# Kernel tuning notes

Hardware: AMD Instinct MI355X
Metric: run time of the kernel (lower is better)

## Reference

```python
import jax, jax.numpy as jnp
from jax import lax
import numpy as np

N_HARMONICS = 8      # matches init_kwargs N
CC_ITERS = 500       # kornia.contrib.connected_components(num_iterations=500)


def _connected_components(mask):
    # kornia-style label propagation: init labels = linear index, bg = 0,
    # iterate 3x3 max-pool restricted to foreground pixels.
    B, C, H, W = mask.shape
    fg = mask == 1.0
    init = jnp.arange(B * C * H * W, dtype=jnp.float32).reshape(B, C, H, W)
    init = jnp.where(fg, init, 0.0)

    def body(_, out):
        pooled = lax.reduce_window(out, -jnp.inf, lax.max,
                                   (1, 1, 3, 3), (1, 1, 1, 1),
                                   ((0, 0), (0, 0), (1, 1), (1, 1)))
        return jnp.where(fg, pooled, out)

    return lax.fori_loop(0, CC_ITERS, body, init)


@jax.jit
def _find_contours(img):
    # img: [B,1,H,W] binary float
    p = jnp.pad(img, ((0, 0), (0, 0), (1, 1), (1, 1)))
    cc = _connected_components(p)[:, :, 1:-1, 1:-1]
    k = jnp.array([[1., 1., 1.], [1., -8., 1.], [1., 1., 1.]], jnp.float32)[None, None]
    conv = lax.conv_general_dilated(p, k, (1, 1), ((1, 1), (1, 1)),
                                    dimension_numbers=('NCHW', 'OIHW', 'NCHW'))
    boundary = (conv < 0).astype(jnp.float32)[:, :, 1:-1, 1:-1]
    return boundary * cc  # labeled contour image


def _components_np(img, N):
    # Per unique label (incl. 0, exactly as torch.unique does): sort points by
    # polar angle about their centroid, compute Fourier amplitudes A[1..N].
    centers, amps = [], []
    for lab in np.unique(img):
        pts = np.argwhere(img == lab).astype(np.float32)  # (row, col), row-major like torch.nonzero
        c = pts.mean(axis=0)
        ang = np.arctan2(pts[:, 1] - c[1], pts[:, 0] - c[0])
        pts = pts[np.argsort(ang, kind='stable')]
        p2 = np.roll(pts, -1, axis=0)
        d1 = np.sqrt((pts[:, 1] - c[1]) ** 2 + (pts[:, 0] - c[0]) ** 2)
        d2 = np.sqrt((p2[:, 1] - c[1]) ** 2 + (p2[:, 0] - c[0]) ** 2)
        delta = d1 - d2
        d3 = np.sqrt(((pts - p2) ** 2).sum(-1))
        l = np.cumsum(d3)
        L = l[-1] if l[-1] != 0 else 1.0
        nz = delta != 0
        k = np.arange(1, N + 1, dtype=np.float32)[:, None]          # [N,1]
        ph = 2.0 * np.pi * k * l[nz][None, :] / L                    # [N,M]
        a = (delta[nz][None] * np.sin(ph)).sum(-1) / (k[:, 0] * np.pi)
        b = -(delta[nz][None] * np.cos(ph)).sum(-1) / (k[:, 0] * np.pi)
        amps.append(np.sqrt(a * a + b * b).astype(np.float32))
        centers.append(c)
    return np.stack(centers), np.stack(amps)


def _pairs(pred_c, tgt_c, N):
    # Geometry preprocessing (integer coords -> constants): per batch item,
    # amplitudes for pred/gt objects plus nearest-centroid matching.
    out = []
    for b in range(pred_c.shape[0]):
        pi, ti = pred_c[b, 0], tgt_c[b, 0]
        if ti.sum() == 0 or pi.sum() == 0:
            out.append(None)
            continue
        p_cent, pA = _components_np(pi, N)
        g_cent, gA = _components_np(ti, N)
        if g_cent.shape[0] <= p_cent.shape[0]:
            d = np.linalg.norm(g_cent[:, None] - p_cent[None], axis=-1)
            out.append((pA, gA, d.argmin(axis=1), True))
        else:
            d = np.linalg.norm(p_cent[:, None] - g_cent[None], axis=-1)
            out.append((pA, gA, d.argmin(axis=1), False))
    return out


def _loss_from_pairs(pairs, weight):
    scale = 0.5 * weight ** 2
    shift = jnp.log(1.0 + weight ** 2)
    total = jnp.zeros((), jnp.float32)
    for pr in pairs:
        if pr is None:
            continue
        pA, gA, m, gt_le = pr
        pd = jnp.asarray(pA) * scale + shift
        gd = jnp.asarray(gA) * scale + shift
        diff = jnp.abs(pd[m] - gd) if gt_le else jnp.abs(gd[m] - pd)
        total = total + diff.sum()
    return total


def setup_inputs() -> dict:
    key = jax.random.key(0)
    B, H, W = 2, 512, 512
    base = np.zeros((H, W), np.float32)
    for i in range(8):
        for j in range(8):
            base[20 + i * 60:56 + i * 60, 20 + j * 60:56 + j * 60] = 1.0
    target = np.broadcast_to(base, (B, 1, H, W)).copy()
    pred_mask = np.stack([np.roll(base, 3 * (b + 1), axis=1) for b in range(B)])[:, None]
    noise = np.asarray(jax.random.normal(key, (B, 1, H, W), jnp.float32))
    pred = 4.0 * pred_mask - 2.0 + 0.05 * noise  # logits; never flips threshold
    return {"pred": jnp.asarray(pred, jnp.float32),
            "target": jnp.asarray(target, jnp.float32),
            "weight": jnp.ones((), jnp.float32)}


def reference(pred, target, weight):
    predm = (jax.nn.sigmoid(pred) > 0.5).astype(jnp.float32)
    if target.ndim == 3:
        target = target[:, None]
    pc = np.asarray(_find_contours(predm))
    tc = np.asarray(_find_contours(target))
    pairs = _pairs(pc, tc, N_HARMONICS)
    return _loss_from_pairs(pairs, weight)
```

## Files before the change

### kernel.cpp

```cpp
#include <hip/hip_runtime.h>
#include <cstdint>
#include <cstddef>

#pragma clang fp contract(off)

#define DEVFN __device__ __forceinline__

constexpr int H = 512, W = 512, HW = H * W;
constexpr int NIMG = 4;
constexpr int PADW = 514;
constexpr int PADHW = PADW * PADW;
constexpr int MAXC = 128;
constexpr int NH = 8;
constexpr int PADCAP = 2 * HW;
constexpr int LEAFCAP = 6144;
constexpr int BMW = 16520;
constexpr int PROP_ITERS = 6;
constexpr int TILE = 2048;
constexpr int PSTRIDE = HW + 4 * MAXC;

constexpr float TWOPIF = (float)(2.0 * 3.14159265358979323846);
constexpr float PIF    = (float)(3.14159265358979323846);

struct Ptrs {
  const float* pred; const float* tgt; const float* wgt; float* out;
  int *labA, *labB, *cid;
  unsigned *pts, *sortPts, *bitmap;
  unsigned long long *keys;
  int *lablist, *counts, *offs, *aoffs, *poffs, *plog, *ptot, *ncomp;
  int *RC, *mcnt, *leafCnt, *leafBase, *leafTot, *leaves, *mergecnt;
  float *dpt, *sortD, *Lval, *centers, *leafSums, *amps;
  float2 *pair;
  float2 *nz;
};

DEVFN int point_search(const int* offs, int nc, int p) {
  int lo = 0, hi = nc - 1;
  while (lo < hi) { int mid = (lo + hi + 1) >> 1; if (offs[mid] <= p) lo = mid; else hi = mid - 1; }
  return lo;
}
DEVFN int seg_search(const int* poffs, const int* plog, int nc, int s) {
  int lo = 0, hi = nc - 1;
  while (lo < hi) { int mid = (lo + hi + 1) >> 1; if (poffs[mid] <= s) lo = mid; else hi = mid - 1; }
  if (s < poffs[lo] + (1 << plog[lo])) return lo;
  return -1;
}

__global__ void k_init(Ptrs w) {
  int idx = blockIdx.x * blockDim.x + threadIdx.x;
  if (idx >= NIMG * HW) return;
  int img = idx / HW, p = idx % HW, r = p / W, c = p % W;
  bool fg;
  if (img < 2) fg = w.pred[img * HW + p] > 0.0f;
  else         fg = (w.tgt[(img - 2) * HW + p] == 1.0f);
  int b = img & 1;
  w.labA[idx] = fg ? (b * PADHW + (r + 1) * PADW + (c + 1)) : 0;
}

__global__ void k_prop(const int* src, int* dst) {
  int idx = blockIdx.x * blockDim.x + threadIdx.x;
  if (idx >= NIMG * HW) return;
  int img = idx / HW, p = idx % HW, r = p / W, c = p % W;
  const int* s = src + img * HW;
  int own = s[p];
  if (own <= 0) { dst[idx] = own; return; }
  int best = own;
  for (int dr = -1; dr <= 1; dr++)
    for (int dc = -1; dc <= 1; dc++) {
      int rr = r + dr, cc2 = c + dc;
      if (rr < 0 || rr >= H || cc2 < 0 || cc2 >= W) continue;
      int v = s[rr * W + cc2];
      if (v > best) best = v;
    }
  int b = img & 1;
  int rel = best - b * PADHW;
  int qr = rel / PADW - 1, qc = rel % PADW - 1;
  int v2 = s[qr * W + qc];
  if (v2 > best) best = v2;
  dst[idx] = best;
}

__global__ void k_contour(Ptrs w) {
  int idx = blockIdx.x * blockDim.x + threadIdx.x;
  if (idx >= NIMG * HW) return;
  int img = idx / HW, p = idx % HW, r = p / W, c = p % W;
  const int* lab = w.labA + img * HW;
  int lv = lab[p];
  int outv = 0;
  if (lv > 0) {
    bool bg = false;
    for (int dr = -1; dr <= 1 && !bg; dr++)
      for (int dc = -1; dc <= 1; dc++) {
        if (dr == 0 && dc == 0) continue;
        int rr = r + dr, cc2 = c + dc;
        bool nfg = (rr >= 0 && rr < H && cc2 >= 0 && cc2 < W) ? (lab[rr * W + cc2] > 0) : false;
        if (!nfg) { bg = true; break; }
      }
    if (bg) outv = lv;
  }
  w.labB[idx] = outv;
}

__global__ void k_bitmap(Ptrs w) {
  int idx = blockIdx.x * blockDim.x + threadIdx.x;
  if (idx >= NIMG * HW) return;
  int img = idx / HW;
  int v = w.labB[idx];
  int lane = threadIdx.x & 63;
  int prev = __shfl_up(v, 1);
  if (lane == 0 || v != prev)
    atomicOr(&w.bitmap[img * BMW + (v >> 5)], 1u << (v & 31));
}

__global__ void k_collect(Ptrs w) {
  int idx = blockIdx.x * blockDim.x + threadIdx.x;
  if (idx >= NIMG * BMW) return;
  int img = idx / BMW, wd = idx % BMW;
  unsigned bits = w.bitmap[img * BMW + wd];
  while (bits) {
    int b = __ffs(bits) - 1;
    bits &= bits - 1;
    int slot = atomicAdd(&w.ncomp[img], 1);
    if (slot < MAXC) w.lablist[img * MAXC + slot] = wd * 32 + b;
  }
}
__global__ void k_sortlab(Ptrs w) {
  int img = threadIdx.x; if (img >= NIMG) return;
  int nc = w.ncomp[img];
  if (nc > MAXC) { nc = MAXC; w.ncomp[img] = MAXC; }
  int* ll = w.lablist + img * MAXC;
  for (int a = 1; a < nc; a++) {
    int v = ll[a]; int b = a - 1;
    while (b >= 0 && ll[b] > v) { ll[b + 1] = ll[b]; b--; }
    ll[b + 1] = v;
  }
}

__global__ void k_cid(Ptrs w) {
  int idx = blockIdx.x * blockDim.x + threadIdx.x;
  if (idx >= NIMG * HW) return;
  int img = idx / HW;
  int v = w.labB[idx];
  const int* ll = w.lablist + img * MAXC;
  int nc = w.ncomp[img];
  int lo = 0, hi = nc - 1, c = 0;
  while (lo <= hi) {
    int mid = (lo + hi) >> 1; int lv = ll[mid];
    if (lv == v) { c = mid; break; }
    if (lv < v) lo = mid + 1; else hi = mid - 1;
  }
  w.cid[idx] = c;
}

__global__ void k_rowcount(Ptrs w) {
  __shared__ int cnt[64 * MAXC];
  int t = threadIdx.x;
  int rowg = blockIdx.x * 64 + t;
  for (int j = 0; j < MAXC; j++) cnt[t * MAXC + j] = 0;
  int img = rowg / H, r = rowg % H;
  for (int c = 0; c < W; c++) cnt[t * MAXC + w.cid[img * HW + r * W + c]]++;
  for (int j = 0; j < MAXC; j++) w.RC[rowg * MAXC + j] = cnt[t * MAXC + j];
}
__global__ void k_colsum(Ptrs w) {
  int idx = blockIdx.x * blockDim.x + threadIdx.x;
  if (idx >= NIMG * MAXC) return;
  int img = idx / MAXC, comp = idx % MAXC;
  const int* rcp = w.RC + (size_t)img * H * MAXC + comp;
  int s = 0;
  #pragma unroll 8
  for (int r = 0; r < H; r++) s += rcp[(size_t)r * MAXC];
  w.counts[img * MAXC + comp] = s;
}
__global__ void k_offsets(Ptrs w) {
  int img = threadIdx.x; if (img >= NIMG) return;
  int nc = w.ncomp[img];
  int* offs  = w.offs  + img * (MAXC + 1);
  int* aoffs = w.aoffs + img * (MAXC + 1);
  int* poffs = w.poffs + img * (MAXC + 1);
  int* plog  = w.plog  + img * MAXC;
  const int* counts = w.counts + img * MAXC;
  int acc = 0, po = 0, ao = 0;
  for (int c = 0; c < nc; c++) {
    offs[c] = acc; acc += counts[c];
    aoffs[c] = ao; ao += (counts[c] + 3) & ~3;
    int n = counts[c];
    int lg = 0; while ((1 << lg) < n) lg++;
    int P = 1 << lg;
    po = (po + P - 1) & ~(P - 1);
    poffs[c] = po; plog[c] = lg; po += P;
  }
  offs[nc] = acc; aoffs[nc] = ao; poffs[nc] = po;
  w.ptot[img] = po;
}
__global__ void k_rowscan(Ptrs w) {
  int idx = blockIdx.x * blockDim.x + threadIdx.x;
  if (idx >= NIMG * MAXC) return;
  int img = idx / MAXC, comp = idx % MAXC;
  if (comp >= w.ncomp[img]) return;
  int base = w.offs[img * (MAXC + 1) + comp];
  for (int r = 0; r < H; r++) {
    int row = img * H + r;
    int tmp = w.RC[row * MAXC + comp];
    w.RC[row * MAXC + comp] = base;
    base += tmp;
  }
}
__global__ void k_scatter(Ptrs w) {
  __shared__ int run[64 * MAXC];
  int t = threadIdx.x;
  int rowg = blockIdx.x * 64 + t;
  for (int j = 0; j < MAXC; j++) run[t * MAXC + j] = w.RC[rowg * MAXC + j];
  int img = rowg / H, r = rowg % H;
  float* planeR = (float*)w.labA + img * HW;
  float* planeC = (float*)w.labB + img * HW;
  for (int c = 0; c < W; c++) {
    int v = w.cid[img * HW + r * W + c];
    int pos = run[t * MAXC + v]++;
    w.pts[img * HW + pos] = ((unsigned)r << 16) | (unsigned)c;
    planeR[pos] = (float)r;
    planeC[pos] = (float)c;
  }
}

__global__ __launch_bounds__(192, 1) void k_mean(Ptrs w) {
  __shared__ alignas(16) float rbuf[2][TILE];
  __shared__ alignas(16) float cbuf[2][TILE];
  int bid = blockIdx.x;
  int img = bid / MAXC, comp = bid % MAXC;
  if (comp >= w.ncomp[img]) return;
  int n = w.counts[img * MAXC + comp];
  int base = w.offs[img * (MAXC + 1) + comp];
  const float* srcR = (const float*)w.labA + img * HW + base;
  const float* srcC = (const float*)w.labB + img * HW + base;
  int t = threadIdx.x;
  int ntile = (n + TILE - 1) / TILE;

  auto fill = [&](int tl, int bb, int lo, int step) {
    int tb = tl * TILE;
    int len = n - tb; if (len > TILE) len = TILE;
    for (int j = lo; j < len; j += step) {
      rbuf[bb][j] = srcR[tb + j];
      cbuf[bb][j] = srcC[tb + j];
    }
  };

  fill(0, 0, t, 192);
  __syncthreads();
  float s = 0.f;
  for (int tl = 0; tl < ntile; tl++) {
    int bb = tl & 1;
    if (t >= 64 && tl + 1 < ntile) fill(tl + 1, bb ^ 1, t - 64, 128);
    if (t < 2) {
      const float*  fb = (t == 0) ? &rbuf[bb][0] : &cbuf[bb][0];
      const float4* b4 = (const float4*)fb;
      int len = n - tl * TILE; if (len > TILE) len = TILE;
      int nb = len >> 6;
      for (int b = 0; b < nb; b++) {
        const float4* _s = b4 + (size_t)b * 16;
        float4 A0=_s[0],A1=_s[1],A2=_s[2],A3=_s[3],A4=_s[4],A5=_s[5],A6=_s[6],A7=_s[7];
        float4 A8=_s[8],A9=_s[9],A10=_s[10],A11=_s[11],A12=_s[12],A13=_s[13],A14=_s[14],A15=_s[15];
        s=s+A0.x; s=s+A0.y; s=s+A0.z; s=s+A0.w;  s=s+A1.x; s=s+A1.y; s=s+A1.z; s=s+A1.w;
        s=s+A2.x; s=s+A2.y; s=s+A2.z; s=s+A2.w;  s=s+A3.x; s=s+A3.y; s=s+A3.z; s=s+A3.w;
        s=s+A4.x; s=s+A4.y; s=s+A4.z; s=s+A4.w;  s=s+A5.x; s=s+A5.y; s=s+A5.z; s=s+A5.w;
        s=s+A6.x; s=s+A6.y; s=s+A6.z; s=s+A6.w;  s=s+A7.x; s=s+A7.y; s=s+A7.z; s=s+A7.w;
        s=s+A8.x; s=s+A8.y; s=s+A8.z; s=s+A8.w;  s=s+A9.x; s=s+A9.y; s=s+A9.z; s=s+A9.w;
        s=s+A10.x;s=s+A10.y;s=s+A10.z;s=s+A10.w; s=s+A11.x;s=s+A11.y;s=s+A11.z;s=s+A11.w;
        s=s+A12.x;s=s+A12.y;s=s+A12.z;s=s+A12.w; s=s+A13.x;s=s+A13.y;s=s+A13.z;s=s+A13.w;
        s=s+A14.x;s=s+A14.y;s=s+A14.z;s=s+A14.w; s=s+A15.x;s=s+A15.y;s=s+A15.z;s=s+A15.w;
      }
      for (int j = nb << 6; j < len; j++) s = s + fb[j];
    }
    __syncthreads();
  }
  float sr = __shfl(s, 0);
  float sc = __shfl(s, 1);
  if (t == 0) {
    w.centers[(img * MAXC + comp) * 2 + 0] = (float)((double)sr / (double)n);
    w.centers[(img * MAXC + comp) * 2 + 1] = (float)((double)sc / (double)n);
  }
}

__global__ void k_keys(Ptrs w) {
  int idx = blockIdx.x * blockDim.x + threadIdx.x;
  if (idx >= NIMG * PADCAP) return;
  int img = idx / PADCAP, s = idx % PADCAP;
  unsigned long long key = ~0ULL;
  int nc = w.ncomp[img];
  const int* poffs = w.poffs + img * (MAXC + 1);
  const int* plog  = w.plog  + img * MAXC;
  if (s < w.ptot[img]) {
    int comp = seg_search(poffs, plog, nc, s);
    if (comp >= 0) {
      int li = s - poffs[comp];
      int n = w.counts[img * MAXC + comp];
      if (li < n) {
        int pbase = w.offs[img * (MAXC + 1) + comp];
        unsigned u = w.pts[img * HW + pbase + li];
        float rowf = (float)(u >> 16), colf = (float)(u & 0xFFFFu);
        float cr = w.centers[(img * MAXC + comp) * 2 + 0];
        float cc = w.centers[(img * MAXC + comp) * 2 + 1];
        float dy = colf - cc;
        float dx = rowf - cr;
        float ang = (float)atan2((double)dy, (double)dx);
        float q1 = dy * dy;
        float q2 = dx * dx;
        float ss = q1 + q2;
        w.dpt[img * HW + pbase + li] = sqrtf(ss);
        unsigned bits = __float_as_uint(ang);
        unsigned k32 = (bits & 0x80000000u) ? ~bits : (bits | 0x80000000u);
        key = ((unsigned long long)k32 << 32) | (unsigned)li;
      }
    }
  }
  w.keys[img * PADCAP + s] = key;
}

__global__ void k_bitonic_local(Ptrs w, int mode, int sizeLog) {
  __shared__ unsigned long long sk[2048];
  __shared__ int   sli[2048];
  __shared__ short scomp[2048];
  __shared__ short spl[2048];
  int tilesPerImg = PADCAP / 2048;
  int img = blockIdx.x / tilesPerImg;
  int tb = (blockIdx.x % tilesPerImg) * 2048;
  int pt = w.ptot[img];
  if (tb >= pt) return;
  const int* poffs = w.poffs + img * (MAXC + 1);
  const int* plog  = w.plog  + img * MAXC;
  int nc = w.ncomp[img];
  for (int u = threadIdx.x; u < 2048; u += blockDim.x) {
    int s = tb + u;
    sk[u] = w.keys[img * PADCAP + s];
    int comp = (s < pt) ? seg_search(poffs, plog, nc, s) : -1;
    scomp[u] = (short)comp;
    spl[u] = comp >= 0 ? (short)plog[comp] : (short)-1;
    sli[u] = comp >= 0 ? s - poffs[comp] : 0;
  }
  __syncthreads();
  int t = threadIdx.x;
  int slLo, slHi;
  if (mode == 0) { slLo = 1; slHi = 11; } else { slLo = sizeLog; slHi = sizeLog; }
  for (int sl = slLo; sl <= slHi; sl++) {
    int size = 1 << sl;
    int stTop = (mode == 0) ? (sl - 1) : 10;
    for (int st = stTop; st >= 0; st--) {
      int stride = 1 << st;
      int i = ((t >> st) << (st + 1)) | (t & (stride - 1));
      int j = i + stride;
      if (scomp[i] >= 0 && scomp[i] == scomp[j] && sl <= spl[i]) {
        bool asc = ((sli[i] & size) == 0);
        if ((sk[i] > sk[j]) == asc) {
          unsigned long long tmp = sk[i]; sk[i] = sk[j]; sk[j] = tmp;
        }
      }
      __syncthreads();
    }
  }
  for (int u = threadIdx.x; u < 2048; u += blockDim.x) w.keys[img * PADCAP + tb + u] = sk[u];
}

__global__ void k_bitonic_global(Ptrs w, int sizeLog, int strideLog) {
  int idx = blockIdx.x * blockDim.x + threadIdx.x;
  const int half = 1 << 17;
  if (idx >= NIMG * half) return;
  int img = idx / half, tt = idx % half;
  int stride = 1 << strideLog;
  int i = ((tt >> strideLog) << (strideLog + 1)) | (tt & (stride - 1));
  int j = i + stride;
  int pt = w.ptot[img];
  if (i >= pt) return;
  const int* poffs = w.poffs + img * (MAXC + 1);
  const int* plog  = w.plog  + img * MAXC;
  int nc = w.ncomp[img];
  int ci = seg_search(poffs, plog, nc, i);
  int cj = (j < pt) ? seg_search(poffs, plog, nc, j) : -1;
  if (ci < 0 || ci != cj) return;
  if (sizeLog > plog[ci]) return;
  bool asc = (((i - poffs[ci]) & (1 << sizeLog)) == 0);
  unsigned long long a = w.keys[img * PADCAP + i];
  unsigned long long b = w.keys[img * PADCAP + j];
  if ((a > b) == asc) {
    w.keys[img * PADCAP + i] = b;
    w.keys[img * PADCAP + j] = a;
  }
}

__global__ void k_gather_sorted(Ptrs w) {
  int idx = blockIdx.x * blockDim.x + threadIdx.x;
  if (idx >= NIMG * HW) return;
  int img = idx / HW, p = idx % HW;
  const int* offs = w.offs + img * (MAXC + 1);
  int comp = point_search(offs, w.ncomp[img], p);
  int li = p - offs[comp];
  int slot = w.poffs[img * (MAXC + 1) + comp] + li;
  unsigned long long key = w.keys[img * PADCAP + slot];
  int rank = (int)(unsigned)(key & 0xFFFFFFFFULL);
  w.sortPts[idx] = w.pts[img * HW + offs[comp] + rank];
  w.sortD[idx]   = w.dpt[img * HW + offs[comp] + rank];
}

__global__ void k_delta(Ptrs w) {
  int idx = blockIdx.x * blockDim.x + threadIdx.x;
  if (idx >= NIMG * HW) return;
  int img = idx / HW, p = idx % HW;
  const int* offs = w.offs + img * (MAXC + 1);
  int comp = point_search(offs, w.ncomp[img], p);
  int li = p - offs[comp];
  int n = w.counts[img * MAXC + comp];
  int jn = (li + 1 < n) ? (p + 1) : offs[comp];
  int jn_abs = img * HW + jn;
  float dlt = w.sortD[idx] - w.sortD[jn_abs];
  unsigned u = w.sortPts[idx], v = w.sortPts[jn_abs];
  float dr = (float)(int)(u >> 16) - (float)(int)(v >> 16);
  float dc = (float)(int)(u & 0xFFFFu) - (float)(int)(v & 0xFFFFu);
  float q1 = dr * dr;
  float q2 = dc * dc;
  float ss = q1 + q2;
  int ai = img * PSTRIDE + w.aoffs[img * (MAXC + 1) + comp] + li;
  w.pair[ai] = make_float2(sqrtf(ss), dlt);
}

__global__ __launch_bounds__(256, 1) void k_cumsum(Ptrs w) {
  __shared__ alignas(16) float dbuf[3][TILE];
  __shared__ alignas(16) float tbuf[3][TILE];
  __shared__ alignas(16) float lbuf[2][TILE];
  int bid = blockIdx.x;
  int img = bid / MAXC, comp = bid % MAXC;
  if (comp >= w.ncomp[img]) return;
  int n = w.counts[img * MAXC + comp];
  int base = w.offs[img * (MAXC + 1) + comp];
  int abase = w.aoffs[img * (MAXC + 1) + comp];
  const float2* pr = w.pair + (size_t)img * PSTRIDE + abase;
  float2* nzp = w.nz + img * HW + base;
  int t = threadIdx.x;
  int lane3 = t - 192;
  int ntile = (n + TILE - 1) / TILE;
  float l = 0.f;
  int mcur = 0;

  auto fill = [&](int tl, int lo, int step) {
    int cb = tl % 3;
    int tb = tl * TILE;
    int len = n - tb; if (len > TILE) len = TILE;
    const float2* src = pr + tb;
    for (int j = lo; j < len; j += step) {
      float2 p = src[j];
      dbuf[cb][j] = p.x;
      tbuf[cb][j] = p.y;
    }
  };

  auto compact = [&](int tlc) {
    int cb = tlc % 3, lb = tlc & 1;
    int tb = tlc * TILE;
    int len = n - tb; if (len > TILE) len = TILE;
    const float* tv = tbuf[cb];
    const float* lv = lbuf[lb];
    int nblk = (len + 63) >> 6;
    for (int b = 0; b < nblk; b++) {
      int j = (b << 6) + lane3;
      float dv = (j < len) ? tv[j] : 0.0f;
      bool nz = (j < len) && (dv != 0.0f);
      unsigned long long mask = __ballot(nz);
      int pos = mcur + __popcll(mask & ((1ull << lane3) - 1ull));
      if (nz) nzp[pos] = make_float2(dv, lv[j]);
      mcur += __popcll(mask);
    }
  };

  fill(0, t, 256);
  __syncthreads();
  for (int tl = 0; tl < ntile; tl++) {
    int cb = tl % 3;
    if (t >= 64 && t < 192) {
      if (tl + 1 < ntile) fill(tl + 1, t - 64, 128);
    } else if (t == 0) {
      int len = n - tl * TILE; if (len > TILE) len = TILE;
      const float4* d4 = (const float4*)&dbuf[cb][0];
      float*  lbr = lbuf[tl & 1];
      float4* lb4 = (float4*)lbr;
      int nb = len >> 6;
      for (int b = 0; b < nb; b++) {
        const float4* _s = d4 + (size_t)b * 16;
        float4 A0=_s[0],A1=_s[1],A2=_s[2],A3=_s[3],A4=_s[4],A5=_s[5],A6=_s[6],A7=_s[7];
        float4 A8=_s[8],A9=_s[9],A10=_s[10],A11=_s[11],A12=_s[12],A13=_s[13],A14=_s[14],A15=_s[15];
        float4* _d = lb4 + (size_t)b * 16;
        float4 L;
        l=l+A0.x; L.x=l; l=l+A0.y; L.y=l; l=l+A0.z; L.z=l; l=l+A0.w; L.w=l; _d[0]=L;
        l=l+A1.x; L.x=l; l=l+A1.y; L.y=l; l=l+A1.z; L.z=l; l=l+A1.w; L.w=l; _d[1]=L;
        l=l+A2.x; L.x=l; l=l+A2.y; L.y=l; l=l+A2.z; L.z=l; l=l+A2.w; L.w=l; _d[2]=L;
        l=l+A3.x; L.x=l; l=l+A3.y; L.y=l; l=l+A3.z; L.z=l; l=l+A3.w; L.w=l; _d[3]=L;
        l=l+A4.x; L.x=l; l=l+A4.y; L.y=l; l=l+A4.z; L.z=l; l=l+A4.w; L.w=l; _d[4]=L;
        l=l+A5.x; L.x=l; l=l+A5.y; L.y=l; l=l+A5.z; L.z=l; l=l+A5.w; L.w=l; _d[5]=L;
        l=l+A6.x; L.x=l; l=l+A6.y; L.y=l; l=l+A6.z; L.z=l; l=l+A6.w; L.w=l; _d[6]=L;
        l=l+A7.x; L.x=l; l=l+A7.y; L.y=l; l=l+A7.z; L.z=l; l=l+A7.w; L.w=l; _d[7]=L;
        l=l+A8.x; L.x=l; l=l+A8.y; L.y=l; l=l+A8.z; L.z=l; l=l+A8.w; L.w=l; _d[8]=L;
        l=l+A9.x; L.x=l; l=l+A9.y; L.y=l; l=l+A9.z; L.z=l; l=l+A9.w; L.w=l; _d[9]=L;
        l=l+A10.x; L.x=l; l=l+A10.y; L.y=l; l=l+A10.z; L.z=l; l=l+A10.w; L.w=l; _d[10]=L;
        l=l+A11.x; L.x=l; l=l+A11.y; L.y=l; l=l+A11.z; L.z=l; l=l+A11.w; L.w=l; _d[11]=L;
        l=l+A12.x; L.x=l; l=l+A12.y; L.y=l; l=l+A12.z; L.z=l; l=l+A12.w; L.w=l; _d[12]=L;
        l=l+A13.x; L.x=l; l=l+A13.y; L.y=l; l=l+A13.z; L.z=l; l=l+A13.w; L.w=l; _d[13]=L;
        l=l+A14.x; L.x=l; l=l+A14.y; L.y=l; l=l+A14.z; L.z=l; l=l+A14.w; L.w=l; _d[14]=L;
        l=l+A15.x; L.x=l; l=l+A15.y; L.y=l; l=l+A15.z; L.z=l; l=l+A15.w; L.w=l; _d[15]=L;
      }
      for (int j = nb << 6; j < len; j++) {
        l = l + dbuf[cb][j];
        lbr[j] = l;
      }
    } else if (t >= 192 && tl > 0) {
      compact(tl - 1);
    }
    __syncthreads();
  }
  if (t >= 192) compact(ntile - 1);
  if (t == 192) w.mcnt[img * MAXC + comp] = mcur;
  if (t == 0)  w.Lval[img * MAXC + comp] = (l != 0.0f) ? l : 1.0f;
}

__global__ __launch_bounds__(128) void k_leafcount(Ptrs w) {
  __shared__ int sN[40][128];
  int img = blockIdx.x;
  int t = threadIdx.x, comp = t;
  if (comp >= w.ncomp[img]) return;
  int m = w.mcnt[img * MAXC + comp];
  int cnt = 0;
  if (m > 0) {
    int sp = 0, n = m;
    for (;;) {
      while (n > 128) { int n2 = n / 2; n2 -= n2 % 8; sN[sp][t] = n - n2; sp++; n = n2; }
      cnt++;
      if (sp == 0) break;
      sp--; n = sN[sp][t];
    }
  }
  w.leafCnt[img * MAXC + comp] = cnt;
}
__global__ void k_leafscan(Ptrs w) {
  int img = threadIdx.x; if (img >= NIMG) return;
  int nc = w.ncomp[img];
  int base = 0;
  for (int c = 0; c < nc; c++) {
    w.leafBase[img * MAXC + c] = base;
    base += w.leafCnt[img * MAXC + c];
  }
  w.leafTot[img] = base <= LEAFCAP ? base : LEAFCAP;
}
__global__ __launch_bounds__(128) void k_leaffill(Ptrs w) {
  __shared__ int sS[32][128], sN[32][128], sR[32][128];
  int img = blockIdx.x;
  int t = threadIdx.x, comp = t;
  if (comp >= w.ncomp[img]) return;
  int m = w.mcnt[img * MAXC + comp];
  if (m <= 0) return;
  int pbase = w.offs[img * (MAXC + 1) + comp];
  int pos = w.leafBase[img * MAXC + comp];
  int sp = 0, s = 0, n = m, rc = 0, prevv = 0;
  for (;;) {
    while (n > 128) {
      int n2 = n / 2; n2 -= n2 % 8;
      sS[sp][t] = s + n2; sN[sp][t] = n - n2; sR[sp][t] = rc + 1; sp++;
      n = n2;
    }
    if (pos < LEAFCAP) {
      int* e = &w.leaves[(img * LEAFCAP + pos) * 3];
      e[0] = pbase + s; e[1] = n; e[2] = comp;
      if (pos > w.leafBase[img * MAXC + comp])
        w.mergecnt[img * LEAFCAP + pos - 1] = prevv + 1 - rc;
    }
    prevv = rc; pos++;
    if (sp == 0) break;
    sp--; s = sS[sp][t]; n = sN[sp][t]; rc = sR[sp][t];
  }
  if (pos - 1 < LEAFCAP) w.mergecnt[img * LEAFCAP + pos - 1] = prevv;
}

DEVFN void leaf_term(const Ptrs& w, int img, int at, float pk, float Lv, float& ta, float& tb) {
  float2 p = w.nz[img * HW + at];
  float t1 = pk * p.y;
  float ph = t1 / Lv;
  double sd, cd;
  sincos((double)ph, &sd, &cd);
  ta = p.x * (float)sd;
  tb = p.x * (float)cd;
}

__global__ void k_leafsums(Ptrs w) {
  int idx = blockIdx.x * blockDim.x + threadIdx.x;
  if (idx >= NIMG * NH * LEAFCAP) return;
  int img = idx / (NH * LEAFCAP);
  int rem = idx % (NH * LEAFCAP);
  int k = rem / LEAFCAP, li = rem % LEAFCAP;
  if (li >= w.leafTot[img]) return;
  const int* e = &w.leaves[(img * LEAFCAP + li) * 3];
  int start = e[0], len = e[1], comp = e[2];
  float Lv = w.Lval[img * MAXC + comp];
  float kf = (float)(k + 1);
  float pk = TWOPIF * kf;
  float A, B;
  if (len < 8) {
    float ra = 0.f, rb = 0.f;
    for (int i = 0; i < len; i++) { float ta, tb; leaf_term(w, img, start + i, pk, Lv, ta, tb); ra += ta; rb += tb; }
    A = ra; B = rb;
  } else {
    float ra[8], rb[8];
    for (int j = 0; j < 8; j++) leaf_term(w, img, start + j, pk, Lv, ra[j], rb[j]);
    int lim = len - (len % 8);
    int i = 8;
    for (; i < lim; i += 8)
      for (int j = 0; j < 8; j++) { float ta, tb; leaf_term(w, img, start + i + j, pk, Lv, ta, tb); ra[j] += ta; rb[j] += tb; }
    float resa = ((ra[0] + ra[1]) + (ra[2] + ra[3])) + ((ra[4] + ra[5]) + (ra[6] + ra[7]));
    float resb = ((rb[0] + rb[1]) + (rb[2] + rb[3])) + ((rb[4] + rb[5]) + (rb[6] + rb[7]));
    for (; i < len; i++) { float ta, tb; leaf_term(w, img, start + i, pk, Lv, ta, tb); resa += ta; resb += tb; }
    A = resa; B = resb;
  }
  float* LS = w.leafSums + ((size_t)(img * NH + k) * LEAFCAP + li) * 2;
  LS[0] = A; LS[1] = B;
}

__global__ __launch_bounds__(64) void k_combine(Ptrs w) {
  __shared__ float sA[24][64], sB[24][64];
  int idx = blockIdx.x * 64 + threadIdx.x;
  int t = threadIdx.x;
  if (idx >= NIMG * MAXC * NH) return;
  int img = idx / (MAXC * NH);
  int rem = idx % (MAXC * NH);
  int comp = rem / NH, k = rem % NH;
  if (comp >= w.ncomp[img]) return;
  int m = w.mcnt[img * MAXC + comp];
  float A = 0.f, B = 0.f;
  if (m > 0) {
    int nleaf = w.leafCnt[img * MAXC + comp];
    int cur = w.leafBase[img * MAXC + comp];
    const float2* LS2 = (const float2*)w.leafSums + (size_t)(img * NH + k) * LEAFCAP;
    const int* mcp = w.mergecnt + img * LEAFCAP;
    float2 nxt = LS2[cur]; int nmc = mcp[cur];
    int sp = 0;
    for (int li = 0; li < nleaf; li++) {
      float2 cv = nxt; int mc = nmc;
      if (li + 1 < nleaf) { nxt = LS2[cur + li + 1]; nmc = mcp[cur + li + 1]; }
      float a = cv.x, b = cv.y;
      for (int q = 0; q < mc; q++) { sp--; a = sA[sp][t] + a; b = sB[sp][t] + b; }
      sA[sp][t] = a; sB[sp][t] = b; sp++;
    }
    A = sA[0][t]; B = sB[0][t];
  }
  float kf = (float)(k + 1);
  float denom = kf * PIF;
  float a = A / denom;
  float bb = B / denom;
  float b = -bb;
  float q1 = a * a;
  float q2 = b * b;
  float ssum = q1 + q2;
  w.amps[(img * MAXC + comp) * NH + k] = sqrtf(ssum);
}

__global__ void k_loss(Ptrs w) {
  float wv = w.wgt[0];
  float w2 = wv * wv;
  float scale = 0.5f * w2;
  float shift = (float)log((double)(1.0f + w2));
  float total = 0.f;
  for (int b = 0; b < 2; b++) {
    int ip = b, it = 2 + b;
    int ncp = w.ncomp[ip], nct = w.ncomp[it];
    if (ncp < 2 || nct < 2) continue;
    const float* cp = w.centers + ip * MAXC * 2;
    const float* ct = w.centers + it * MAXC * 2;
    const float* ap = w.amps + ip * MAXC * NH;
    const float* at = w.amps + it * MAXC * NH;
    if (nct <= ncp) {
      for (int tci = 0; tci < nct; tci++) {
        int m = 0; float best = 3.4e38f;
        for (int pci = 0; pci < ncp; pci++) {
          float dr = ct[tci * 2 + 0] - cp[pci * 2 + 0];
          float dc = ct[tci * 2 + 1] - cp[pci * 2 + 1];
          float q1 = dr * dr, q2 = dc * dc;
          float dist = sqrtf(q1 + q2);
          if (dist < best) { best = dist; m = pci; }
        }
        for (int k = 0; k < NH; k++) {
          float pd = ap[m * NH + k] * scale + shift;
          float gd = at[tci * NH + k] * scale + shift;
          total = total + fabsf(pd - gd);
        }
      }
    } else {
      for (int pci = 0; pci < ncp; pci++) {
        int m = 0; float best = 3.4e38f;
        for (int tci = 0; tci < nct; tci++) {
          float dr = cp[pci * 2 + 0] - ct[tci * 2 + 0];
          float dc = cp[pci * 2 + 1] - ct[tci * 2 + 1];
          float q1 = dr * dr, q2 = dc * dc;
          float dist = sqrtf(q1 + q2);
          if (dist < best) { best = dist; m = tci; }
        }
        for (int k = 0; k < NH; k++) {
          float pd = ap[pci * NH + k] * scale + shift;
          float gd = at[m * NH + k] * scale + shift;
          total = total + fabsf(gd - pd);
        }
      }
    }
  }
  w.out[0] = total;
}

__global__ void k_fail(float* out) { out[0] = -12345.0f; }

extern "C" void kernel_launch(void* const* d_in, const int* in_sizes, int n_in,
                              void* d_out, int out_size, void* d_ws, size_t ws_size,
                              hipStream_t stream) {
  (void)in_sizes; (void)n_in; (void)out_size;
  Ptrs w;
  w.pred = (const float*)d_in[0];
  w.tgt  = (const float*)d_in[1];
  w.wgt  = (const float*)d_in[2];
  w.out  = (float*)d_out;

  char* base = (char*)d_ws;
  size_t off = 0;
  auto alloc = [&](size_t nbytes) -> void* {
    off = (off + 255) & ~(size_t)255;
    void* p = base + off;
    off += nbytes;
    return p;
  };
  w.labA    = (int*)alloc((size_t)NIMG * HW * 4 + 512);
  w.labB    = (int*)alloc((size_t)NIMG * HW * 4 + 512);
  w.cid     = (int*)alloc((size_t)NIMG * HW * 4);
  w.pts     = (unsigned*)alloc((size_t)NIMG * HW * 4 + 512);
  w.sortPts = (unsigned*)alloc((size_t)NIMG * HW * 4);
  w.bitmap  = (unsigned*)alloc((size_t)NIMG * BMW * 4);
  w.keys    = (unsigned long long*)alloc((size_t)NIMG * PADCAP * 8);
  w.lablist = (int*)alloc((size_t)NIMG * MAXC * 4);
  w.counts  = (int*)alloc((size_t)NIMG * MAXC * 4);
  w.offs    = (int*)alloc((size_t)NIMG * (MAXC + 1) * 4);
  w.aoffs   = (int*)alloc((size_t)NIMG * (MAXC + 1) * 4);
  w.poffs   = (int*)alloc((size_t)NIMG * (MAXC + 1) * 4);
  w.plog    = (int*)alloc((size_t)NIMG * MAXC * 4);
  w.ptot    = (int*)alloc((size_t)NIMG * 4);
  w.ncomp   = (int*)alloc((size_t)NIMG * 4);
  w.RC      = (int*)alloc((size_t)NIMG * H * MAXC * 4);
  w.mcnt    = (int*)alloc((size_t)NIMG * MAXC * 4);
  w.leafCnt = (int*)alloc((size_t)NIMG * MAXC * 4);
  w.leafBase= (int*)alloc((size_t)NIMG * MAXC * 4);
  w.leafTot = (int*)alloc((size_t)NIMG * 4);
  w.leaves  = (int*)alloc((size_t)NIMG * LEAFCAP * 3 * 4);
  w.mergecnt= (int*)alloc((size_t)NIMG * LEAFCAP * 4);
  w.dpt     = (float*)alloc((size_t)NIMG * HW * 4);
  w.sortD   = (float*)alloc((size_t)NIMG * HW * 4);
  w.pair    = (float2*)alloc((size_t)NIMG * PSTRIDE * 8 + 1024);
  w.nz      = (float2*)alloc((size_t)NIMG * HW * 8);
  w.Lval    = (float*)alloc((size_t)NIMG * MAXC * 4);
  w.centers = (float*)alloc((size_t)NIMG * MAXC * 2 * 4);
  w.leafSums= (float*)alloc((size_t)NIMG * NH * LEAFCAP * 2 * 4);
  w.amps    = (float*)alloc((size_t)NIMG * MAXC * NH * 4);

  if (off > ws_size) {
    hipLaunchKernelGGL(k_fail, dim3(1), dim3(1), 0, stream, (float*)d_out);
    return;
  }

  hipMemsetAsync(w.bitmap, 0, (size_t)NIMG * BMW * 4, stream);
  hipMemsetAsync(w.ncomp, 0, (size_t)NIMG * 4, stream);

  const int NPIX = NIMG * HW;
  dim3 b256(256);
  dim3 gPix((NPIX + 255) / 256);

  hipLaunchKernelGGL(k_init, gPix, b256, 0, stream, w);
  for (int i = 0; i < PROP_ITERS; i++) {
    const int* src = (i & 1) ? w.labB : w.labA;
    int* dst       = (i & 1) ? w.labA : w.labB;
    hipLaunchKernelGGL(k_prop, gPix, b256, 0, stream, src, dst);
  }
  hipLaunchKernelGGL(k_contour, gPix, b256, 0, stream, w);
  hipLaunchKernelGGL(k_bitmap, gPix, b256, 0, stream, w);
  hipLaunchKernelGGL(k_collect, dim3((NIMG * BMW + 255) / 256), b256, 0, stream, w);
  hipLaunchKernelGGL(k_sortlab, dim3(1), dim3(NIMG), 0, stream, w);
  hipLaunchKernelGGL(k_cid, gPix, b256, 0, stream, w);
  hipLaunchKernelGGL(k_rowcount, dim3(NIMG * H / 64), dim3(64), 0, stream, w);
  hipLaunchKernelGGL(k_colsum, dim3((NIMG * MAXC + 255) / 256), b256, 0, stream, w);
  hipLaunchKernelGGL(k_offsets, dim3(1), dim3(NIMG), 0, stream, w);
  hipLaunchKernelGGL(k_rowscan, dim3((NIMG * MAXC + 255) / 256), b256, 0, stream, w);
  hipLaunchKernelGGL(k_scatter, dim3(NIMG * H / 64), dim3(64), 0, stream, w);
  hipLaunchKernelGGL(k_mean, dim3(NIMG * MAXC), dim3(192), 0, stream, w);
  hipLaunchKernelGGL(k_keys, dim3((NIMG * PADCAP + 255) / 256), b256, 0, stream, w);

  dim3 gLoc(NIMG * (PADCAP / 2048));
  dim3 bLoc(1024);
  hipLaunchKernelGGL(k_bitonic_local, gLoc, bLoc, 0, stream, w, 0, 0);
  dim3 gGlob((NIMG * (1 << 17) + 255) / 256);
  for (int sizeLog = 12; sizeLog <= 18; sizeLog++) {
    for (int strideLog = sizeLog - 1; strideLog >= 11; strideLog--)
      hipLaunchKernelGGL(k_bitonic_global, gGlob, b256, 0, stream, w, sizeLog, strideLog);
    hipLaunchKernelGGL(k_bitonic_local, gLoc, bLoc, 0, stream, w, 1, sizeLog);
  }

  hipLaunchKernelGGL(k_gather_sorted, gPix, b256, 0, stream, w);
  hipLaunchKernelGGL(k_delta, gPix, b256, 0, stream, w);
  hipLaunchKernelGGL(k_cumsum, dim3(NIMG * MAXC), b256, 0, stream, w);
  hipLaunchKernelGGL(k_leafcount, dim3(NIMG), dim3(128), 0, stream, w);
  hipLaunchKernelGGL(k_leafscan, dim3(1), dim3(NIMG), 0, stream, w);
  hipLaunchKernelGGL(k_leaffill, dim3(NIMG), dim3(128), 0, stream, w);
  hipLaunchKernelGGL(k_leafsums, dim3((NIMG * NH * LEAFCAP + 255) / 256), b256, 0, stream, w);
  hipLaunchKernelGGL(k_combine, dim3((NIMG * MAXC * NH + 63) / 64), dim3(64), 0, stream, w);
  hipLaunchKernelGGL(k_loss, dim3(1), dim3(1), 0, stream, w);
}
```

Measured before the change: 6.096 ms.

## Fuse pairs of bitonic global stages and software-pipeline LDS reads in serial scans

Adds a bitonic kernel that performs two consecutive global merge stages (stride 2^st and 2^(st-1)) on four elements per thread. This halves the number of global passes and launches over the key array for the large-stride steps. The serial sum and cumsum loops in k_mean and k_cumsum are also double-buffered, so the next 64-float block is loaded from LDS while the current one is accumulated, hiding shared-memory latency on the single-thread chain. The fused kernel still runs four segment searches per thread, and the double buffering raises register pressure.

```diff
diff --git a/kernel.cpp b/kernel.cpp
--- a/kernel.cpp
+++ b/kernel.cpp
@@ -222,6 +222,16 @@
   }
 }
 
+#define LD16(P, BASE, S) { const float4* _s = (BASE) + (size_t)(S) * 16; \
+  P##0 = _s[0];  P##1 = _s[1];  P##2 = _s[2];  P##3 = _s[3]; \
+  P##4 = _s[4];  P##5 = _s[5];  P##6 = _s[6];  P##7 = _s[7]; \
+  P##8 = _s[8];  P##9 = _s[9];  P##10 = _s[10]; P##11 = _s[11]; \
+  P##12 = _s[12]; P##13 = _s[13]; P##14 = _s[14]; P##15 = _s[15]; }
+#define SUM4(Q) { s = s + (Q).x; s = s + (Q).y; s = s + (Q).z; s = s + (Q).w; }
+#define SUM64(P) { SUM4(P##0) SUM4(P##1) SUM4(P##2) SUM4(P##3) SUM4(P##4) SUM4(P##5) SUM4(P##6) SUM4(P##7) \
+  SUM4(P##8) SUM4(P##9) SUM4(P##10) SUM4(P##11) SUM4(P##12) SUM4(P##13) SUM4(P##14) SUM4(P##15) }
+#define DEC16(P) float4 P##0,P##1,P##2,P##3,P##4,P##5,P##6,P##7,P##8,P##9,P##10,P##11,P##12,P##13,P##14,P##15;
+
 __global__ __launch_bounds__(192, 1) void k_mean(Ptrs w) {
   __shared__ alignas(16) float rbuf[2][TILE];
   __shared__ alignas(16) float cbuf[2][TILE];
@@ -255,18 +265,17 @@
       const float4* b4 = (const float4*)fb;
       int len = n - tl * TILE; if (len > TILE) len = TILE;
       int nb = len >> 6;
-      for (int b = 0; b < nb; b++) {
-        const float4* _s = b4 + (size_t)b * 16;
-        float4 A0=_s[0],A1=_s[1],A2=_s[2],A3=_s[3],A4=_s[4],A5=_s[5],A6=_s[6],A7=_s[7];
-        float4 A8=_s[8],A9=_s[9],A10=_s[10],A11=_s[11],A12=_s[12],A13=_s[13],A14=_s[14],A15=_s[15];
-        s=s+A0.x; s=s+A0.y; s=s+A0.z; s=s+A0.w;  s=s+A1.x; s=s+A1.y; s=s+A1.z; s=s+A1.w;
-        s=s+A2.x; s=s+A2.y; s=s+A2.z; s=s+A2.w;  s=s+A3.x; s=s+A3.y; s=s+A3.z; s=s+A3.w;
-        s=s+A4.x; s=s+A4.y; s=s+A4.z; s=s+A4.w;  s=s+A5.x; s=s+A5.y; s=s+A5.z; s=s+A5.w;
-        s=s+A6.x; s=s+A6.y; s=s+A6.z; s=s+A6.w;  s=s+A7.x; s=s+A7.y; s=s+A7.z; s=s+A7.w;
-        s=s+A8.x; s=s+A8.y; s=s+A8.z; s=s+A8.w;  s=s+A9.x; s=s+A9.y; s=s+A9.z; s=s+A9.w;
-        s=s+A10.x;s=s+A10.y;s=s+A10.z;s=s+A10.w; s=s+A11.x;s=s+A11.y;s=s+A11.z;s=s+A11.w;
-        s=s+A12.x;s=s+A12.y;s=s+A12.z;s=s+A12.w; s=s+A13.x;s=s+A13.y;s=s+A13.z;s=s+A13.w;
-        s=s+A14.x;s=s+A14.y;s=s+A14.z;s=s+A14.w; s=s+A15.x;s=s+A15.y;s=s+A15.z;s=s+A15.w;
+      DEC16(A) DEC16(B)
+      int b = 0;
+      if (nb > 0) { LD16(A, b4, 0); }
+      while (b < nb) {
+        if (b + 1 < nb) { LD16(B, b4, b + 1); }
+        SUM64(A);
+        b++;
+        if (b >= nb) break;
+        if (b + 1 < nb) { LD16(A, b4, b + 1); }
+        SUM64(B);
+        b++;
       }
       for (int j = nb << 6; j < len; j++) s = s + fb[j];
     }
@@ -385,6 +394,52 @@
   }
 }
 
+__global__ void k_bitonic_global2(Ptrs w, int sizeLog, int stHi) {
+  int idx = blockIdx.x * blockDim.x + threadIdx.x;
+  const int quarter = 1 << 16;
+  if (idx >= NIMG * quarter) return;
+  int img = idx / quarter, tt = idx % quarter;
+  int s1 = 1 << stHi, s0 = s1 >> 1;
+  int e0 = ((tt >> (stHi - 1)) << (stHi + 1)) | (tt & (s0 - 1));
+  int e1 = e0 + s0, e2 = e0 + s1, e3 = e2 + s0;
+  int pt = w.ptot[img];
+  if (e0 >= pt) return;
+  const int* poffs = w.poffs + img * (MAXC + 1);
+  const int* plog  = w.plog  + img * MAXC;
+  int nc = w.ncomp[img];
+  int c0 = seg_search(poffs, plog, nc, e0);
+  int c1 = (e1 < pt) ? seg_search(poffs, plog, nc, e1) : -1;
+  int c2 = (e2 < pt) ? seg_search(poffs, plog, nc, e2) : -1;
+  int c3 = (e3 < pt) ? seg_search(poffs, plog, nc, e3) : -1;
+  unsigned long long* K = w.keys + (size_t)img * PADCAP;
+  unsigned long long k0 = 0, k1 = 0, k2 = 0, k3 = 0;
+  if (e0 < pt) k0 = K[e0];
+  if (e1 < pt) k1 = K[e1];
+  if (e2 < pt) k2 = K[e2];
+  if (e3 < pt) k3 = K[e3];
+  int size = 1 << sizeLog;
+  if (c0 >= 0 && c0 == c2 && sizeLog <= plog[c0]) {
+    bool asc = (((e0 - poffs[c0]) & size) == 0);
+    if ((k0 > k2) == asc) { unsigned long long tm = k0; k0 = k2; k2 = tm; }
+  }
+  if (c1 >= 0 && c1 == c3 && sizeLog <= plog[c1]) {
+    bool asc = (((e1 - poffs[c1]) & size) == 0);
+    if ((k1 > k3) == asc) { unsigned long long tm = k1; k1 = k3; k3 = tm; }
+  }
+  if (c0 >= 0 && c0 == c1 && sizeLog <= plog[c0]) {
+    bool asc = (((e0 - poffs[c0]) & size) == 0);
+    if ((k0 > k1) == asc) { unsigned long long tm = k0; k0 = k1; k1 = tm; }
+  }
+  if (c2 >= 0 && c2 == c3 && sizeLog <= plog[c2]) {
+    bool asc = (((e2 - poffs[c2]) & size) == 0);
+    if ((k2 > k3) == asc) { unsigned long long tm = k2; k2 = k3; k3 = tm; }
+  }
+  if (e0 < pt) K[e0] = k0;
+  if (e1 < pt) K[e1] = k1;
+  if (e2 < pt) K[e2] = k2;
+  if (e3 < pt) K[e3] = k3;
+}
+
 __global__ void k_gather_sorted(Ptrs w) {
   int idx = blockIdx.x * blockDim.x + threadIdx.x;
   if (idx >= NIMG * HW) return;
@@ -420,6 +475,14 @@
   w.pair[ai] = make_float2(sqrtf(ss), dlt);
 }
 
+#define CH4(Q, D, I) { float4 L; \
+  l = l + (Q).x; L.x = l; l = l + (Q).y; L.y = l; \
+  l = l + (Q).z; L.z = l; l = l + (Q).w; L.w = l; (D)[I] = L; }
+#define CHN64(P, S) { float4* _d = lb4 + (size_t)(S) * 16; \
+  CH4(P##0,_d,0)  CH4(P##1,_d,1)  CH4(P##2,_d,2)  CH4(P##3,_d,3) \
+  CH4(P##4,_d,4)  CH4(P##5,_d,5)  CH4(P##6,_d,6)  CH4(P##7,_d,7) \
+  CH4(P##8,_d,8)  CH4(P##9,_d,9)  CH4(P##10,_d,10) CH4(P##11,_d,11) \
+  CH4(P##12,_d,12) CH4(P##13,_d,13) CH4(P##14,_d,14) CH4(P##15,_d,15) }
 __global__ __launch_bounds__(256, 1) void k_cumsum(Ptrs w) {
   __shared__ alignas(16) float dbuf[3][TILE];
   __shared__ alignas(16) float tbuf[3][TILE];
@@ -480,28 +543,17 @@
       float*  lbr = lbuf[tl & 1];
       float4* lb4 = (float4*)lbr;
       int nb = len >> 6;
-      for (int b = 0; b < nb; b++) {
-        const float4* _s = d4 + (size_t)b * 16;
-        float4 A0=_s[0],A1=_s[1],A2=_s[2],A3=_s[3],A4=_s[4],A5=_s[5],A6=_s[6],A7=_s[7];
-        float4 A8=_s[8],A9=_s[9],A10=_s[10],A11=_s[11],A12=_s[12],A13=_s[13],A14=_s[14],A15=_s[15];
-        float4* _d = lb4 + (size_t)b * 16;
-        float4 L;
-        l=l+A0.x; L.x=l; l=l+A0.y; L.y=l; l=l+A0.z; L.z=l; l=l+A0.w; L.w=l; _d[0]=L;
-        l=l+A1.x; L.x=l; l=l+A1.y; L.y=l; l=l+A1.z; L.z=l; l=l+A1.w; L.w=l; _d[1]=L;
-        l=l+A2.x; L.x=l; l=l+A2.y; L.y=l; l=l+A2.z; L.z=l; l=l+A2.w; L.w=l; _d[2]=L;
-        l=l+A3.x; L.x=l; l=l+A3.y; L.y=l; l=l+A3.z; L.z=l; l=l+A3.w; L.w=l; _d[3]=L;
-        l=l+A4.x; L.x=l; l=l+A4.y; L.y=l; l=l+A4.z; L.z=l; l=l+A4.w; L.w=l; _d[4]=L;
-        l=l+A5.x; L.x=l; l=l+A5.y; L.y=l; l=l+A5.z; L.z=l; l=l+A5.w; L.w=l; _d[5]=L;
-        l=l+A6.x; L.x=l; l=l+A6.y; L.y=l; l=l+A6.z; L.z=l; l=l+A6.w; L.w=l; _d[6]=L;
-        l=l+A7.x; L.x=l; l=l+A7.y; L.y=l; l=l+A7.z; L.z=l; l=l+A7.w; L.w=l; _d[7]=L;
-        l=l+A8.x; L.x=l; l=l+A8.y; L.y=l; l=l+A8.z; L.z=l; l=l+A8.w; L.w=l; _d[8]=L;
-        l=l+A9.x; L.x=l; l=l+A9.y; L.y=l; l=l+A9.z; L.z=l; l=l+A9.w; L.w=l; _d[9]=L;
-        l=l+A10.x; L.x=l; l=l+A10.y; L.y=l; l=l+A10.z; L.z=l; l=l+A10.w; L.w=l; _d[10]=L;
-        l=l+A11.x; L.x=l; l=l+A11.y; L.y=l; l=l+A11.z; L.z=l; l=l+A11.w; L.w=l; _d[11]=L;
-        l=l+A12.x; L.x=l; l=l+A12.y; L.y=l; l=l+A12.z; L.z=l; l=l+A12.w; L.w=l; _d[12]=L;
-        l=l+A13.x; L.x=l; l=l+A13.y; L.y=l; l=l+A13.z; L.z=l; l=l+A13.w; L.w=l; _d[13]=L;
-        l=l+A14.x; L.x=l; l=l+A14.y; L.y=l; l=l+A14.z; L.z=l; l=l+A14.w; L.w=l; _d[14]=L;
-        l=l+A15.x; L.x=l; l=l+A15.y; L.y=l; l=l+A15.z; L.z=l; l=l+A15.w; L.w=l; _d[15]=L;
+      DEC16(A) DEC16(B)
+      int b = 0;
+      if (nb > 0) { LD16(A, d4, 0); }
+      while (b < nb) {
+        if (b + 1 < nb) { LD16(B, d4, b + 1); }
+        CHN64(A, b);
+        b++;
+        if (b >= nb) break;
+        if (b + 1 < nb) { LD16(A, d4, b + 1); }
+        CHN64(B, b);
+        b++;
       }
       for (int j = nb << 6; j < len; j++) {
         l = l + dbuf[cb][j];
@@ -792,9 +844,18 @@
   dim3 bLoc(1024);
   hipLaunchKernelGGL(k_bitonic_local, gLoc, bLoc, 0, stream, w, 0, 0);
   dim3 gGlob((NIMG * (1 << 17) + 255) / 256);
+  dim3 gQuad((NIMG * (1 << 16) + 255) / 256);
   for (int sizeLog = 12; sizeLog <= 18; sizeLog++) {
-    for (int strideLog = sizeLog - 1; strideLog >= 11; strideLog--)
-      hipLaunchKernelGGL(k_bitonic_global, gGlob, b256, 0, stream, w, sizeLog, strideLog);
+    int st = sizeLog - 1;
+    while (st >= 11) {
+      if (st >= 12) {
+        hipLaunchKernelGGL(k_bitonic_global2, gQuad, b256, 0, stream, w, sizeLog, st);
+        st -= 2;
+      } else {
+        hipLaunchKernelGGL(k_bitonic_global, gGlob, b256, 0, stream, w, sizeLog, st);
+        st -= 1;
+      }
+    }
     hipLaunchKernelGGL(k_bitonic_local, gLoc, bLoc, 0, stream, w, 1, sizeLog);
   }
 
```

Measured after the change: 5.939 ms. -2.6%, faster.
